# Kernel tuning notes

Hardware: AMD Instinct MI355X
Metric: run time of the kernel (lower is better)

## Reference

```python
import jax, jax.numpy as jnp
import numpy as np
import math

B, S, H = 8, 160, 768
DEP = 64
NH, DH = 12, H // 12
W_EDGE = 1.0
EPS = 1e-5


def setup_inputs() -> dict:
    key = jax.random.key(0)
    ks = jax.random.split(key, 16)
    sc_h = 1.0 / math.sqrt(H)
    sc_d = 1.0 / math.sqrt(DEP)
    return {
        "token_feature": jax.random.normal(ks[0], (B, S, H), jnp.float32),
        "edge_feature": jax.random.normal(ks[1], (B, S, S, DEP), jnp.float32),
        "dependency_masks": jax.random.randint(ks[2], (B, S, S), 0, 2, jnp.int32),
        "Wq": jax.random.normal(ks[3], (H, H), jnp.float32) * sc_h,
        "bq": jnp.zeros((H,), jnp.float32),
        "Wk": jax.random.normal(ks[4], (H, H), jnp.float32) * sc_h,
        "bk": jnp.zeros((H,), jnp.float32),
        "Wv": jax.random.normal(ks[5], (H, H), jnp.float32) * sc_h,
        "bv": jnp.zeros((H,), jnp.float32),
        "Wek": jax.random.normal(ks[6], (DEP, H), jnp.float32) * sc_d,
        "bek": jnp.zeros((H,), jnp.float32),
        "Wev": jax.random.normal(ks[7], (DEP, H), jnp.float32) * sc_d,
        "bev": jnp.zeros((H,), jnp.float32),
        "ln_g": jnp.ones((H,), jnp.float32),
        "ln_b": jnp.zeros((H,), jnp.float32),
    }


def _heads3(x):  # [B,S,H] -> [B,NH,S,DH]
    return x.reshape(B, S, NH, DH).transpose(0, 2, 1, 3)


def _heads4(x):  # [B,S,S,H] -> [B,NH,S,S,DH]
    return x.reshape(B, S, S, NH, DH).transpose(0, 3, 1, 2, 4)


def reference(token_feature, edge_feature, dependency_masks,
              Wq, bq, Wk, bk, Wv, bv, Wek, bek, Wev, bev, ln_g, ln_b):
    q = _heads3(token_feature @ Wq + bq)   # [B,NH,S,DH]
    k = _heads3(token_feature @ Wk + bk)
    v = _heads3(token_feature @ Wv + bv)
    ek = _heads4(edge_feature @ Wek + bek)  # [B,NH,S,S,DH]
    ev = _heads4(edge_feature @ Wev + bev)
    # key_ij = k_j + w*ek_ij ; scores_ij = q_i . key_ij / sqrt(dh)
    scores = (jnp.einsum('bhid,bhjd->bhij', q, k)
              + W_EDGE * jnp.einsum('bhid,bhijd->bhij', q, ek))
    scores = scores / math.sqrt(DH)
    mask = (dependency_masks[:, None, :, :] == 0)  # [B,1,S,S]
    scores = jnp.where(mask, jnp.float32(-10000.0), scores)
    probs = jax.nn.softmax(scores, axis=-1)  # dropout is identity in eval
    ctx = (jnp.einsum('bhij,bhjd->bhid', probs, v)
           + W_EDGE * jnp.einsum('bhij,bhijd->bhid', probs, ev))
    ctx = ctx.transpose(0, 2, 1, 3).reshape(B, S, H)
    x = token_feature + ctx
    mu = jnp.mean(x, axis=-1, keepdims=True)
    var = jnp.mean(jnp.square(x - mu), axis=-1, keepdims=True)
    return (x - mu) / jnp.sqrt(var + EPS) * ln_g + ln_b
```

## Files before the change

### kernel.cpp

```cpp
#include <hip/hip_runtime.h>
#include <hip/hip_bf16.h>
#include <math.h>

#define BB 8
#define SS 160
#define HH 768
#define DEPTH 64
#define NHEAD 12
#define DHEAD 64
#define BS (BB*SS)
#define SCROW (NHEAD*SS)

constexpr float EPS_C = 1e-5f;

typedef __attribute__((ext_vector_type(8))) short bf16x8;
typedef __attribute__((ext_vector_type(4))) float f32x4;

__device__ inline short f2bs(float x) {
    union { __hip_bfloat16 b; short s; } u;
    u.b = __float2bfloat16(x);
    return u.s;
}

__global__ __launch_bounds__(256) void gemm_qkv(
    const float* __restrict__ X,
    const float* __restrict__ Wq, const float* __restrict__ Wk,
    const float* __restrict__ Wv,
    const float* __restrict__ bq, const float* __restrict__ bk,
    const float* __restrict__ bv,
    __hip_bfloat16* __restrict__ qb, __hip_bfloat16* __restrict__ kb,
    __hip_bfloat16* __restrict__ vb)
{
    __shared__ int4 sA[4][128];
    __shared__ int4 sB[4][64];
    int m0 = blockIdx.x * 128, n0 = blockIdx.y * 64, mat = blockIdx.z;
    const float* W    = (mat == 0) ? Wq : (mat == 1) ? Wk : Wv;
    const float* bias = (mat == 0) ? bq : (mat == 1) ? bk : bv;
    int tid = threadIdx.x, w = tid >> 6, l = tid & 63;
    int wm = (w >> 1) * 64, wn = (w & 1) * 32;
    int khalf = l >> 4, lc = l & 15;

    f32x4 acc[4][2];
#pragma unroll
    for (int i = 0; i < 4; i++)
#pragma unroll
        for (int j = 0; j < 2; j++) acc[i][j] = (f32x4){0.f, 0.f, 0.f, 0.f};

    for (int k0 = 0; k0 < HH; k0 += 32) {
        __syncthreads();
#pragma unroll
        for (int rr = 0; rr < 2; rr++) {
            const float* ap = X + (size_t)(m0 + l + rr * 64) * HH + k0 + w * 8;
            float4 x0 = *(const float4*)ap;
            float4 x1 = *(const float4*)(ap + 4);
            bf16x8 p;
            p[0]=f2bs(x0.x); p[1]=f2bs(x0.y); p[2]=f2bs(x0.z); p[3]=f2bs(x0.w);
            p[4]=f2bs(x1.x); p[5]=f2bs(x1.y); p[6]=f2bs(x1.z); p[7]=f2bs(x1.w);
            *(bf16x8*)&sA[w][l + rr * 64] = p;
        }
        {
            const float* wp = W + (size_t)(k0 + w * 8) * HH + n0 + l;
            bf16x8 p;
#pragma unroll
            for (int i = 0; i < 8; i++) p[i] = f2bs(wp[(size_t)i * HH]);
            *(bf16x8*)&sB[w][l] = p;
        }
        __syncthreads();
        bf16x8 b0 = *(const bf16x8*)&sB[khalf][wn + lc];
        bf16x8 b1 = *(const bf16x8*)&sB[khalf][wn + 16 + lc];
#pragma unroll
        for (int mi = 0; mi < 4; mi++) {
            bf16x8 a = *(const bf16x8*)&sA[khalf][wm + mi * 16 + lc];
            acc[mi][0] = __builtin_amdgcn_mfma_f32_16x16x32_bf16(a, b0, acc[mi][0], 0, 0, 0);
            acc[mi][1] = __builtin_amdgcn_mfma_f32_16x16x32_bf16(a, b1, acc[mi][1], 0, 0, 0);
        }
    }

    int rg = (l >> 4) * 4;
    __hip_bfloat16* outm = (mat == 0) ? qb : (mat == 1) ? kb : vb;
#pragma unroll
    for (int ni = 0; ni < 2; ni++) {
        int gcol = n0 + wn + ni * 16 + lc;
        float bv_ = bias[gcol];
#pragma unroll
        for (int mi = 0; mi < 4; mi++) {
            int grow = m0 + wm + mi * 16 + rg;
            f32x4 a = acc[mi][ni];
            __hip_bfloat16* o = outm + (size_t)grow * HH + gcol;
            o[0]      = __float2bfloat16(a.x + bv_);
            o[HH]     = __float2bfloat16(a.y + bv_);
            o[2 * HH] = __float2bfloat16(a.z + bv_);
            o[3 * HH] = __float2bfloat16(a.w + bv_);
        }
    }
}

__global__ __launch_bounds__(256) void scores_gemm(
    const __hip_bfloat16* __restrict__ qb, const __hip_bfloat16* __restrict__ kb,
    _Float16* __restrict__ sc)
{
    __shared__ int4 sQ[8][160];
    __shared__ int4 sK[8][160];
    int h = blockIdx.x, b = blockIdx.y;
    const short* Q = (const short*)qb + (size_t)b * SS * HH + h * DHEAD;
    const short* K = (const short*)kb + (size_t)b * SS * HH + h * DHEAD;
    int tid = threadIdx.x, w = tid >> 6, l = tid & 63;

    for (int idx = tid; idx < SS * 8; idx += 256) {
        int row = idx >> 3, ch = idx & 7;
        sQ[ch][row] = *(const int4*)(Q + (size_t)row * HH + ch * 8);
        sK[ch][row] = *(const int4*)(K + (size_t)row * HH + ch * 8);
    }
    __syncthreads();

    int wm = (w >> 1) * 80, wn = (w & 1) * 80;
    int khalf = l >> 4, lc = l & 15;
    f32x4 acc[5][5];
#pragma unroll
    for (int i = 0; i < 5; i++)
#pragma unroll
        for (int j = 0; j < 5; j++) acc[i][j] = (f32x4){0.f, 0.f, 0.f, 0.f};

#pragma unroll
    for (int s = 0; s < 2; s++) {
        int c = s * 4 + khalf;
        bf16x8 bf[5];
#pragma unroll
        for (int ni = 0; ni < 5; ni++)
            bf[ni] = *(const bf16x8*)&sK[c][wn + ni * 16 + lc];
#pragma unroll
        for (int mi = 0; mi < 5; mi++) {
            bf16x8 a = *(const bf16x8*)&sQ[c][wm + mi * 16 + lc];
#pragma unroll
            for (int ni = 0; ni < 5; ni++)
                acc[mi][ni] = __builtin_amdgcn_mfma_f32_16x16x32_bf16(a, bf[ni], acc[mi][ni], 0, 0, 0);
        }
    }

    int rg = (l >> 4) * 4;
    _Float16* base = sc + ((size_t)b * SS) * SCROW + (size_t)h * SS;
#pragma unroll
    for (int mi = 0; mi < 5; mi++) {
        int i0 = wm + mi * 16 + rg;
#pragma unroll
        for (int ni = 0; ni < 5; ni++) {
            int j = wn + ni * 16 + lc;
            f32x4 a = acc[mi][ni];
            base[(size_t)(i0 + 0) * SCROW + j] = (_Float16)(a.x * 0.125f);
            base[(size_t)(i0 + 1) * SCROW + j] = (_Float16)(a.y * 0.125f);
            base[(size_t)(i0 + 2) * SCROW + j] = (_Float16)(a.z * 0.125f);
            base[(size_t)(i0 + 3) * SCROW + j] = (_Float16)(a.w * 0.125f);
        }
    }
}

__global__ __launch_bounds__(256) void qek_slim(
    const __hip_bfloat16* __restrict__ qb, const float* __restrict__ Wek,
    __hip_bfloat16* __restrict__ qek)
{
    __shared__ short sW[8 * 65 * 8];
    int h = blockIdx.x, mg = blockIdx.y;
    int tid = threadIdx.x, w = tid >> 6, l = tid & 63;
    int lr = l & 15, kg = l >> 4;

    {
        int d = tid >> 2, q4 = tid & 3;
        const float* wp = Wek + (size_t)d * HH + h * DHEAD + q4 * 16;
        float4 w0 = *(const float4*)(wp);
        float4 w1 = *(const float4*)(wp + 4);
        float4 w2 = *(const float4*)(wp + 8);
        float4 w3 = *(const float4*)(wp + 12);
        bf16x8 p0, p1;
        p0[0]=f2bs(w0.x); p0[1]=f2bs(w0.y); p0[2]=f2bs(w0.z); p0[3]=f2bs(w0.w);
        p0[4]=f2bs(w1.x); p0[5]=f2bs(w1.y); p0[6]=f2bs(w1.z); p0[7]=f2bs(w1.w);
        p1[0]=f2bs(w2.x); p1[1]=f2bs(w2.y); p1[2]=f2bs(w2.z); p1[3]=f2bs(w2.w);
        p1[4]=f2bs(w3.x); p1[5]=f2bs(w3.y); p1[6]=f2bs(w3.z); p1[7]=f2bs(w3.w);
        *(bf16x8*)&sW[((q4 * 2) * 65 + d) * 8]     = p0;
        *(bf16x8*)&sW[((q4 * 2 + 1) * 65 + d) * 8] = p1;
    }
    __syncthreads();

    bf16x8 bfrag[2][4];
#pragma unroll
    for (int s = 0; s < 2; s++)
#pragma unroll
        for (int nt = 0; nt < 4; nt++)
            bfrag[s][nt] = *(const bf16x8*)&sW[((s * 4 + kg) * 65 + nt * 16 + lr) * 8];

    const short* Q = (const short*)qb;
    short* O = (short*)qek;
    int m0 = (mg * 4 + w) * 16;
    bf16x8 a0 = *(const bf16x8*)(Q + (size_t)(m0 + lr) * HH + h * DHEAD + kg * 8);
    bf16x8 a1 = *(const bf16x8*)(Q + (size_t)(m0 + lr) * HH + h * DHEAD + 32 + kg * 8);
#pragma unroll
    for (int nt = 0; nt < 4; nt++) {
        f32x4 acc = (f32x4){0.f, 0.f, 0.f, 0.f};
        acc = __builtin_amdgcn_mfma_f32_16x16x32_bf16(a0, bfrag[0][nt], acc, 0, 0, 0);
        acc = __builtin_amdgcn_mfma_f32_16x16x32_bf16(a1, bfrag[1][nt], acc, 0, 0, 0);
        int row0 = m0 + kg * 4;
#pragma unroll
        for (int r = 0; r < 4; r++)
            O[(size_t)(row0 + r) * HH + h * DHEAD + nt * 16 + lr] = f2bs(acc[r]);
    }
}

__global__ __launch_bounds__(256) void escore_add2(
    const float* __restrict__ edge, const __hip_bfloat16* __restrict__ qek,
    _Float16* __restrict__ sc)
{
    int task = blockIdx.x * 4 + (threadIdx.x >> 6);
    int l = threadIdx.x & 63;
    int bi = task / 5, seg = task - (task / 5) * 5;
    int lr = l & 15, kg = l >> 4;

    const short* QE = (const short*)qek + (size_t)bi * HH;
    bf16x8 qe0 = *(const bf16x8*)(QE + lr * DHEAD + kg * 8);
    bf16x8 qe1 = *(const bf16x8*)(QE + lr * DHEAD + 32 + kg * 8);

    const float* E = edge + (size_t)bi * SS * DEPTH;
    _Float16* srow = sc + (size_t)bi * SCROW;

#pragma unroll
    for (int t = 0; t < 2; t++) {
        int jt = seg * 2 + t;
        const float* ep = E + (size_t)(jt * 16 + lr) * DEPTH + kg * 8;
        float4 e0 = *(const float4*)(ep);
        float4 e1 = *(const float4*)(ep + 4);
        float4 e2 = *(const float4*)(ep + 32);
        float4 e3 = *(const float4*)(ep + 36);
        bf16x8 a0, a1;
        a0[0]=f2bs(e0.x); a0[1]=f2bs(e0.y); a0[2]=f2bs(e0.z); a0[3]=f2bs(e0.w);
        a0[4]=f2bs(e1.x); a0[5]=f2bs(e1.y); a0[6]=f2bs(e1.z); a0[7]=f2bs(e1.w);
        a1[0]=f2bs(e2.x); a1[1]=f2bs(e2.y); a1[2]=f2bs(e2.z); a1[3]=f2bs(e2.w);
        a1[4]=f2bs(e3.x); a1[5]=f2bs(e3.y); a1[6]=f2bs(e3.z); a1[7]=f2bs(e3.w);
        f32x4 acc = (f32x4){0.f, 0.f, 0.f, 0.f};
        acc = __builtin_amdgcn_mfma_f32_16x16x32_bf16(a0, qe0, acc, 0, 0, 0);
        acc = __builtin_amdgcn_mfma_f32_16x16x32_bf16(a1, qe1, acc, 0, 0, 0);
        if (lr < NHEAD) {
            int j0 = jt * 16 + kg * 4;
            _Float16* p = srow + (size_t)lr * SS + j0;
#pragma unroll
            for (int r = 0; r < 4; r++)
                p[r] = (_Float16)((float)p[r] + 0.125f * acc[r]);
        }
    }
}

__global__ __launch_bounds__(256) void attn_kernel(
    const float* __restrict__ token, const float* __restrict__ edge,
    const int* __restrict__ mask,
    const __hip_bfloat16* __restrict__ q_ws, const _Float16* __restrict__ sc,
    const __hip_bfloat16* __restrict__ v_ws,
    const float* __restrict__ bek,
    const float* __restrict__ Wev, const float* __restrict__ bev,
    const float* __restrict__ ln_g, const float* __restrict__ ln_b,
    float* __restrict__ out)
{
    __shared__ float  s_ctx[HH];
    __shared__ float  s_scores[NHEAD][SS];
    __shared__ float  s_pe[NHEAD][DEPTH];
    __shared__ float  s_x[HH];
    __shared__ float  s_qbek[NHEAD];
    __shared__ int    s_mask[SS];
    __shared__ float  s_red[8];

    int bi = blockIdx.x;
    int b  = bi / SS;
    int tid = threadIdx.x;
    int w = tid >> 6, l = tid & 63;
    int lr = l & 15, kg = l >> 4;

    if (tid < SS) s_mask[tid] = mask[(size_t)bi * SS + tid];

    {
        int hs = w * 3 + kg;
        float part = 0.f;
        if (hs < NHEAD) {
            const __hip_bfloat16* qp = q_ws + (size_t)bi * HH + hs * DHEAD + lr * 4;
            float4 bv4 = *(const float4*)(bek + hs * DHEAD + lr * 4);
            part = __bfloat162float(qp[0]) * bv4.x + __bfloat162float(qp[1]) * bv4.y
                 + __bfloat162float(qp[2]) * bv4.z + __bfloat162float(qp[3]) * bv4.w;
        }
        part += __shfl_xor(part, 1, 64);
        part += __shfl_xor(part, 2, 64);
        part += __shfl_xor(part, 4, 64);
        part += __shfl_xor(part, 8, 64);
        if (lr == 0 && hs < NHEAD) s_qbek[hs] = part;
    }
    __syncthreads();

    const _Float16* scrow = sc + (size_t)bi * SCROW;
    for (int idx = tid; idx < NHEAD * SS; idx += 256) {
        int h = idx / SS, j = idx - h * SS;
        float qk = (float)scrow[idx];
        s_scores[h][j] = s_mask[j] ? (qk + 0.125f * s_qbek[h]) : -10000.0f;
    }
    __syncthreads();

    for (int h = w; h < NHEAD; h += 4) {
        float v0 = s_scores[h][l];
        float v1 = s_scores[h][l + 64];
        float v2 = (l < 32) ? s_scores[h][l + 128] : -INFINITY;
        float mx = fmaxf(v0, fmaxf(v1, v2));
#pragma unroll
        for (int mm = 32; mm >= 1; mm >>= 1) mx = fmaxf(mx, __shfl_xor(mx, mm, 64));
        float e0 = expf(v0 - mx), e1 = expf(v1 - mx);
        float e2 = (l < 32) ? expf(v2 - mx) : 0.f;
        float sm = e0 + e1 + e2;
#pragma unroll
        for (int mm = 32; mm >= 1; mm >>= 1) sm += __shfl_xor(sm, mm, 64);
        float inv = 1.0f / sm;
        s_scores[h][l]      = e0 * inv;
        s_scores[h][l + 64] = e1 * inv;
        if (l < 32) s_scores[h][l + 128] = e2 * inv;
    }
    __syncthreads();

    const float* e_row = edge + (size_t)bi * SS * DEPTH;
    {
        int h0 = w * 3;
        float av0 = 0.f, av1 = 0.f, av2 = 0.f;
        float pe0 = 0.f, pe1 = 0.f, pe2 = 0.f;
        const __hip_bfloat16* vbp = v_ws + (size_t)b * SS * HH + h0 * DHEAD + l;
        const float* er = e_row + l;
        const float* p0r = &s_scores[h0][0];
        const float* p1r = &s_scores[h0 + 1][0];
        const float* p2r = &s_scores[h0 + 2][0];
#pragma unroll 4
        for (int j = 0; j < SS; j++) {
            float p0 = p0r[j], p1 = p1r[j], p2 = p2r[j];
            const __hip_bfloat16* vp = vbp + (size_t)j * HH;
            av0 += p0 * __bfloat162float(vp[0]);
            av1 += p1 * __bfloat162float(vp[DHEAD]);
            av2 += p2 * __bfloat162float(vp[2 * DHEAD]);
            float ev = er[(size_t)j * DEPTH];
            pe0 += p0 * ev; pe1 += p1 * ev; pe2 += p2 * ev;
        }
        s_pe[h0][l]     = pe0;
        s_pe[h0 + 1][l] = pe1;
        s_pe[h0 + 2][l] = pe2;
        s_ctx[h0 * DHEAD + l]       = av0;
        s_ctx[(h0 + 1) * DHEAD + l] = av1;
        s_ctx[(h0 + 2) * DHEAD + l] = av2;
    }
    __syncthreads();

    for (int mdx = tid; mdx < HH; mdx += 256) {
        int h = mdx >> 6;
        const float* pep = &s_pe[h][0];
        float sum = 0.f;
#pragma unroll
        for (int d = 0; d < DEPTH; d++) sum += pep[d] * Wev[(size_t)d * HH + mdx];
        float ctx = s_ctx[mdx] + (sum + bev[mdx]);
        s_x[mdx] = token[(size_t)bi * HH + mdx] + ctx;
    }
    __syncthreads();

    float lsum = 0.f, lsq = 0.f;
    for (int c = tid; c < HH; c += 256) {
        float x = s_x[c];
        lsum += x; lsq += x * x;
    }
#pragma unroll
    for (int mm = 32; mm >= 1; mm >>= 1) {
        lsum += __shfl_xor(lsum, mm, 64);
        lsq  += __shfl_xor(lsq,  mm, 64);
    }
    if (l == 0) { s_red[w] = lsum; s_red[4 + w] = lsq; }
    __syncthreads();
    float tsum = s_red[0] + s_red[1] + s_red[2] + s_red[3];
    float tsq  = s_red[4] + s_red[5] + s_red[6] + s_red[7];
    float mu  = tsum / HH;
    float var = tsq / HH - mu * mu;
    float rstd = rsqrtf(var + EPS_C);
    for (int c = tid; c < HH; c += 256)
        out[(size_t)bi * HH + c] = (s_x[c] - mu) * rstd * ln_g[c] + ln_b[c];
}

extern "C" void kernel_launch(void* const* d_in, const int* in_sizes, int n_in,
                              void* d_out, int out_size, void* d_ws, size_t ws_size,
                              hipStream_t stream) {
    const float* token = (const float*)d_in[0];
    const float* edge  = (const float*)d_in[1];
    const int*   mask  = (const int*)d_in[2];
    const float* Wq = (const float*)d_in[3];  const float* bq = (const float*)d_in[4];
    const float* Wk = (const float*)d_in[5];  const float* bk = (const float*)d_in[6];
    const float* Wv = (const float*)d_in[7];  const float* bv = (const float*)d_in[8];
    const float* Wek = (const float*)d_in[9];  const float* bek = (const float*)d_in[10];
    const float* Wev = (const float*)d_in[11]; const float* bev = (const float*)d_in[12];
    const float* ln_g = (const float*)d_in[13]; const float* ln_b = (const float*)d_in[14];
    float* out = (float*)d_out;

    __hip_bfloat16* qb = (__hip_bfloat16*)d_ws;
    __hip_bfloat16* kb = qb + (size_t)BS * HH;
    __hip_bfloat16* vb = kb + (size_t)BS * HH;
    _Float16*       sc = (_Float16*)(vb + (size_t)BS * HH);
    __hip_bfloat16* qek = kb;

    gemm_qkv<<<dim3(BS / 128, HH / 64, 3), 256, 0, stream>>>(
        token, Wq, Wk, Wv, bq, bk, bv, qb, kb, vb);
    scores_gemm<<<dim3(NHEAD, BB), 256, 0, stream>>>(qb, kb, sc);
    qek_slim<<<dim3(NHEAD, 20), 256, 0, stream>>>(qb, Wek, qek);
    escore_add2<<<1600, 256, 0, stream>>>(edge, qek, sc);
    attn_kernel<<<BS, 256, 0, stream>>>(token, edge, mask, qb, sc, vb,
                                        bek, Wev, bev, ln_g, ln_b, out);
}
```

Measured before the change: 116.9 us.

## Split P·V into per-head MFMA kernel and use MFMA for edge-value reduction

```diff
diff --git a/kernel.cpp b/kernel.cpp
--- a/kernel.cpp
+++ b/kernel.cpp
@@ -246,18 +246,112 @@
     }
 }
 
-__global__ __launch_bounds__(256) void attn_kernel(
+__global__ __launch_bounds__(256) void pv_soft(
+    const __hip_bfloat16* __restrict__ qb, const __hip_bfloat16* __restrict__ vb,
+    const float* __restrict__ bek, const int* __restrict__ mask,
+    const _Float16* __restrict__ sc, __hip_bfloat16* __restrict__ ctxv)
+{
+    __shared__ alignas(16) short sS[SS][168];
+    __shared__ alignas(16) short sVT[DHEAD][168];
+    __shared__ float s_qbek_i[SS];
+    int h = blockIdx.x, b = blockIdx.y;
+    int tid = threadIdx.x, w = tid >> 6, l = tid & 63;
+    int lr = l & 15, kg = l >> 4;
+
+    if (tid < SS) {
+        const __hip_bfloat16* qp = qb + (size_t)(b * SS + tid) * HH + h * DHEAD;
+        const float* bp = bek + h * DHEAD;
+        float s = 0.f;
+#pragma unroll 8
+        for (int c = 0; c < DHEAD; c++) s += __bfloat162float(qp[c]) * bp[c];
+        s_qbek_i[tid] = s;
+    }
+    const short* V = (const short*)vb;
+    for (int idx = tid; idx < SS * DHEAD; idx += 256) {
+        int j = idx >> 6, c = idx & 63;
+        sVT[c][j] = V[(size_t)(b * SS + j) * HH + h * DHEAD + c];
+    }
+    __syncthreads();
+
+    const _Float16* scb = sc + (size_t)b * SS * SCROW + h * SS;
+    const int* mrow = mask + (size_t)b * SS * SS;
+    for (int idx = tid; idx < SS * SS; idx += 256) {
+        int i = idx / SS, j = idx - i * SS;
+        float s = mrow[i * SS + j]
+                ? ((float)scb[(size_t)i * SCROW + j] + 0.125f * s_qbek_i[i])
+                : -10000.f;
+        _Float16 hv = (_Float16)s;
+        sS[i][j] = *(short*)&hv;
+    }
+    __syncthreads();
+
+    for (int r = w; r < SS; r += 4) {
+        _Float16* row = (_Float16*)&sS[r][0];
+        float v0 = (float)row[l];
+        float v1 = (float)row[l + 64];
+        float v2 = (l < 32) ? (float)row[l + 128] : -INFINITY;
+        float mx = fmaxf(v0, fmaxf(v1, v2));
+#pragma unroll
+        for (int mm = 32; mm >= 1; mm >>= 1) mx = fmaxf(mx, __shfl_xor(mx, mm, 64));
+        float e0 = expf(v0 - mx), e1 = expf(v1 - mx);
+        float e2 = (l < 32) ? expf(v2 - mx) : 0.f;
+        float sm = e0 + e1 + e2;
+#pragma unroll
+        for (int mm = 32; mm >= 1; mm >>= 1) sm += __shfl_xor(sm, mm, 64);
+        float inv = 1.0f / sm;
+        sS[r][l]      = f2bs(e0 * inv);
+        sS[r][l + 64] = f2bs(e1 * inv);
+        if (l < 32) sS[r][l + 128] = f2bs(e2 * inv);
+    }
+    __syncthreads();
+
+    int wm = (w >> 1) * 80, wn = (w & 1) * 32;
+    f32x4 acc[5][2];
+#pragma unroll
+    for (int i = 0; i < 5; i++)
+#pragma unroll
+        for (int j = 0; j < 2; j++) acc[i][j] = (f32x4){0.f, 0.f, 0.f, 0.f};
+
+#pragma unroll
+    for (int s = 0; s < 5; s++) {
+        int k0 = s * 32 + kg * 8;
+        bf16x8 b0 = *(const bf16x8*)&sVT[wn + lr][k0];
+        bf16x8 b1 = *(const bf16x8*)&sVT[wn + 16 + lr][k0];
+#pragma unroll
+        for (int mi = 0; mi < 5; mi++) {
+            bf16x8 a = *(const bf16x8*)&sS[wm + mi * 16 + lr][k0];
+            acc[mi][0] = __builtin_amdgcn_mfma_f32_16x16x32_bf16(a, b0, acc[mi][0], 0, 0, 0);
+            acc[mi][1] = __builtin_amdgcn_mfma_f32_16x16x32_bf16(a, b1, acc[mi][1], 0, 0, 0);
+        }
+    }
+
+    short* cv = (short*)ctxv;
+    int rg = kg * 4;
+#pragma unroll
+    for (int ni = 0; ni < 2; ni++) {
+        int c = wn + ni * 16 + lr;
+#pragma unroll
+        for (int mi = 0; mi < 5; mi++) {
+            int i0 = wm + mi * 16 + rg;
+            f32x4 a = acc[mi][ni];
+#pragma unroll
+            for (int r = 0; r < 4; r++)
+                cv[(size_t)(b * SS + i0 + r) * HH + h * DHEAD + c] = f2bs(a[r]);
+        }
+    }
+}
+
+__global__ __launch_bounds__(256) void final_ln(
     const float* __restrict__ token, const float* __restrict__ edge,
     const int* __restrict__ mask,
     const __hip_bfloat16* __restrict__ q_ws, const _Float16* __restrict__ sc,
-    const __hip_bfloat16* __restrict__ v_ws,
+    const __hip_bfloat16* __restrict__ ctxv,
     const float* __restrict__ bek,
     const float* __restrict__ Wev, const float* __restrict__ bev,
     const float* __restrict__ ln_g, const float* __restrict__ ln_b,
     float* __restrict__ out)
 {
-    __shared__ float  s_ctx[HH];
-    __shared__ float  s_scores[NHEAD][SS];
+    __shared__ float  s_scores[NHEAD][SS + 2];
     __shared__ float  s_pe[NHEAD][DEPTH];
     __shared__ float  s_x[HH];
     __shared__ float  s_qbek[NHEAD];
@@ -265,7 +359,6 @@
     __shared__ float  s_red[8];
 
     int bi = blockIdx.x;
-    int b  = bi / SS;
     int tid = threadIdx.x;
     int w = tid >> 6, l = tid & 63;
     int lr = l & 15, kg = l >> 4;
@@ -316,32 +409,27 @@
     }
     __syncthreads();
 
-    const float* e_row = edge + (size_t)bi * SS * DEPTH;
     {
-        int h0 = w * 3;
-        float av0 = 0.f, av1 = 0.f, av2 = 0.f;
-        float pe0 = 0.f, pe1 = 0.f, pe2 = 0.f;
-        const __hip_bfloat16* vbp = v_ws + (size_t)b * SS * HH + h0 * DHEAD + l;
-        const float* er = e_row + l;
-        const float* p0r = &s_scores[h0][0];
-        const float* p1r = &s_scores[h0 + 1][0];
-        const float* p2r = &s_scores[h0 + 2][0];
-#pragma unroll 4
-        for (int j = 0; j < SS; j++) {
-            float p0 = p0r[j], p1 = p1r[j], p2 = p2r[j];
-            const __hip_bfloat16* vp = vbp + (size_t)j * HH;
-            av0 += p0 * __bfloat162float(vp[0]);
-            av1 += p1 * __bfloat162float(vp[DHEAD]);
-            av2 += p2 * __bfloat162float(vp[2 * DHEAD]);
-            float ev = er[(size_t)j * DEPTH];
-            pe0 += p0 * ev; pe1 += p1 * ev; pe2 += p2 * ev;
-        }
-        s_pe[h0][l]     = pe0;
-        s_pe[h0 + 1][l] = pe1;
-        s_pe[h0 + 2][l] = pe2;
-        s_ctx[h0 * DHEAD + l]       = av0;
-        s_ctx[(h0 + 1) * DHEAD + l] = av1;
-        s_ctx[(h0 + 2) * DHEAD + l] = av2;
+        int arow = (lr < NHEAD) ? lr : (NHEAD - 1);
+        const float* Eb = edge + (size_t)bi * SS * DEPTH;
+        int d = w * 16 + lr;
+        f32x4 acc = (f32x4){0.f, 0.f, 0.f, 0.f};
+#pragma unroll
+        for (int s = 0; s < 5; s++) {
+            int k0 = s * 32 + kg * 8;
+            bf16x8 a, bfr;
+#pragma unroll
+            for (int e = 0; e < 8; e++) a[e] = f2bs(s_scores[arow][k0 + e]);
+#pragma unroll
+            for (int e = 0; e < 8; e++)
+                bfr[e] = f2bs(Eb[(size_t)(k0 + e) * DEPTH + d]);
+            acc = __builtin_amdgcn_mfma_f32_16x16x32_bf16(a, bfr, acc, 0, 0, 0);
+        }
+#pragma unroll
+        for (int r = 0; r < 4; r++) {
+            int h = kg * 4 + r;
+            if (h < NHEAD) s_pe[h][d] = acc[r];
+        }
     }
     __syncthreads();
 
@@ -351,8 +439,8 @@
         float sum = 0.f;
 #pragma unroll
         for (int d = 0; d < DEPTH; d++) sum += pep[d] * Wev[(size_t)d * HH + mdx];
-        float ctx = s_ctx[mdx] + (sum + bev[mdx]);
-        s_x[mdx] = token[(size_t)bi * HH + mdx] + ctx;
+        float cvv = __bfloat162float(ctxv[(size_t)bi * HH + mdx]);
+        s_x[mdx] = token[(size_t)bi * HH + mdx] + cvv + sum + bev[mdx];
     }
     __syncthreads();
 
@@ -395,13 +483,15 @@
     __hip_bfloat16* kb = qb + (size_t)BS * HH;
     __hip_bfloat16* vb = kb + (size_t)BS * HH;
     _Float16*       sc = (_Float16*)(vb + (size_t)BS * HH);
-    __hip_bfloat16* qek = kb;
+    __hip_bfloat16* qek  = kb;
+    __hip_bfloat16* ctxv = kb;
 
     gemm_qkv<<<dim3(BS / 128, HH / 64, 3), 256, 0, stream>>>(
         token, Wq, Wk, Wv, bq, bk, bv, qb, kb, vb);
     scores_gemm<<<dim3(NHEAD, BB), 256, 0, stream>>>(qb, kb, sc);
     qek_slim<<<dim3(NHEAD, 20), 256, 0, stream>>>(qb, Wek, qek);
     escore_add2<<<1600, 256, 0, stream>>>(edge, qek, sc);
-    attn_kernel<<<BS, 256, 0, stream>>>(token, edge, mask, qb, sc, vb,
-                                        bek, Wev, bev, ln_g, ln_b, out);
-}
+    pv_soft<<<dim3(NHEAD, BB), 256, 0, stream>>>(qb, vb, bek, mask, sc, ctxv);
+    final_ln<<<BS, 256, 0, stream>>>(token, edge, mask, qb, sc, ctxv,
+                                     bek, Wev, bev, ln_g, ln_b, out);
+}
```

Measured after the change: 182.8 us. 1.56x slower.
